# Optimization experiments

Hardware: AMD Instinct MI355X
Metric: run time of the kernel (lower is better)

The kernel has to match this reference:

```python
import jax, jax.numpy as jnp
import numpy as np

IN_SIZE = 128
OUT_SIZE = 128
NEG_SLOPE = 0.01  # flax.nnx.leaky_relu default negative_slope


def setup_inputs() -> dict:
    key = jax.random.key(0)
    x = jax.random.normal(key, (16, IN_SIZE, IN_SIZE, 128), dtype=jnp.float32)
    return {"x": x}


def reference(x) -> jnp.ndarray:
    B, _, _, C = x.shape
    up = jax.image.resize(x, (B, 2 * IN_SIZE, 2 * IN_SIZE, C), method='bilinear', antialias=False)
    # leaky_relu activation on the enlarged intermediate
    act = jnp.where(up >= 0, up, NEG_SLOPE * up)
    # bilinear downsample back to out_size (antialias=False, matching original)
    out = jax.image.resize(act, (B, OUT_SIZE, OUT_SIZE, C), method='bilinear', antialias=False)
    return out
```

## Files before the change

### kernel.cpp

```cpp
#include <hip/hip_runtime.h>


#define NEG_SLOPE 0.01f

__device__ __forceinline__ float lrelu(float v) {
    return fmaxf(v, NEG_SLOPE * v);
}

__device__ __forceinline__ float stencil(float a, float b, float c,
                                         float d, float e, float f,
                                         float g, float h, float i) {
    float up00 = 0.5625f * e + 0.1875f * (b + d) + 0.0625f * a;
    float up01 = 0.5625f * e + 0.1875f * (b + f) + 0.0625f * c;
    float up10 = 0.5625f * e + 0.1875f * (d + h) + 0.0625f * g;
    float up11 = 0.5625f * e + 0.1875f * (f + h) + 0.0625f * i;
    return 0.25f * (lrelu(up00) + lrelu(up01) + lrelu(up10) + lrelu(up11));
}

__global__ __launch_bounds__(256) void ActivationFilter_kernel(
        const float4* __restrict__ in, float4* __restrict__ out) {
    const int idx = blockIdx.x * 256 + threadIdx.x;
    const int c4 = idx & 31;
    const int x  = (idx >> 5) & 127;
    const int y  = (idx >> 12) & 127;
    const int b  = idx >> 19;

    const int xm = max(x - 1, 0), xp = min(x + 1, 127);
    const int ym = max(y - 1, 0), yp = min(y + 1, 127);

    const int rb = b << 7;
#define LD(Y, X) in[((((rb + (Y)) << 7) + (X)) << 5) + c4]
    const float4 A = LD(ym, xm), B = LD(ym, x), C = LD(ym, xp);
    const float4 D = LD(y,  xm), E = LD(y,  x), F = LD(y,  xp);
    const float4 G = LD(yp, xm), H = LD(yp, x), I = LD(yp, xp);
#undef LD

    float4 o;
    o.x = stencil(A.x, B.x, C.x, D.x, E.x, F.x, G.x, H.x, I.x);
    o.y = stencil(A.y, B.y, C.y, D.y, E.y, F.y, G.y, H.y, I.y);
    o.z = stencil(A.z, B.z, C.z, D.z, E.z, F.z, G.z, H.z, I.z);
    o.w = stencil(A.w, B.w, C.w, D.w, E.w, F.w, G.w, H.w, I.w);

    out[idx] = o;
}

extern "C" void kernel_launch(void* const* d_in, const int* in_sizes, int n_in,
                              void* d_out, int out_size, void* d_ws, size_t ws_size,
                              hipStream_t stream) {
    const float4* in = (const float4*)d_in[0];
    float4* out = (float4*)d_out;
    ActivationFilter_kernel<<<dim3(32768), dim3(256), 0, stream>>>(in, out);
}
```

Baseline: 228.3 us.

## Compute 2x2 output pixels per thread to reuse stencil neighborhood loads

Each thread now loads a 4x4 neighborhood of float4 inputs and produces four adjacent output pixels, instead of loading 9 inputs for a single output. This cuts redundant global/cache load traffic per output from 9 to 4 float4 loads. The launch grid shrinks by 4x to match. The cost is higher register use per thread and fewer threads to hide latency.

```diff
diff --git a/kernel.cpp b/kernel.cpp
--- a/kernel.cpp
+++ b/kernel.cpp
@@ -17,31 +17,46 @@
     return 0.25f * (lrelu(up00) + lrelu(up01) + lrelu(up10) + lrelu(up11));
 }
 
+__device__ __forceinline__ float4 stencil4(const float4& a, const float4& b, const float4& c,
+                                           const float4& d, const float4& e, const float4& f,
+                                           const float4& g, const float4& h, const float4& i) {
+    float4 o;
+    o.x = stencil(a.x, b.x, c.x, d.x, e.x, f.x, g.x, h.x, i.x);
+    o.y = stencil(a.y, b.y, c.y, d.y, e.y, f.y, g.y, h.y, i.y);
+    o.z = stencil(a.z, b.z, c.z, d.z, e.z, f.z, g.z, h.z, i.z);
+    o.w = stencil(a.w, b.w, c.w, d.w, e.w, f.w, g.w, h.w, i.w);
+    return o;
+}
+
 __global__ __launch_bounds__(256) void ActivationFilter_kernel(
         const float4* __restrict__ in, float4* __restrict__ out) {
-    const int idx = blockIdx.x * 256 + threadIdx.x;
-    const int c4 = idx & 31;
-    const int x  = (idx >> 5) & 127;
-    const int y  = (idx >> 12) & 127;
-    const int b  = idx >> 19;
+    const int t  = blockIdx.x * 256 + threadIdx.x;
+    const int c4 = t & 31;
+    const int px = (t >> 5) & 63;
+    const int py = (t >> 11) & 63;
+    const int b  = t >> 17;
 
-    const int xm = max(x - 1, 0), xp = min(x + 1, 127);
-    const int ym = max(y - 1, 0), yp = min(y + 1, 127);
+    const int x0 = px << 1, y0 = py << 1;
+    const int xm = max(x0 - 1, 0), x3 = min(x0 + 2, 127);
+    const int ym = max(y0 - 1, 0), y3 = min(y0 + 2, 127);
 
     const int rb = b << 7;
-#define LD(Y, X) in[((((rb + (Y)) << 7) + (X)) << 5) + c4]
-    const float4 A = LD(ym, xm), B = LD(ym, x), C = LD(ym, xp);
-    const float4 D = LD(y,  xm), E = LD(y,  x), F = LD(y,  xp);
-    const float4 G = LD(yp, xm), H = LD(yp, x), I = LD(yp, xp);
-#undef LD
+#define ADDR(Y, X) (((((rb + (Y)) << 7) + (X)) << 5) + c4)
 
-    float4 o;
-    o.x = stencil(A.x, B.x, C.x, D.x, E.x, F.x, G.x, H.x, I.x);
-    o.y = stencil(A.y, B.y, C.y, D.y, E.y, F.y, G.y, H.y, I.y);
-    o.z = stencil(A.z, B.z, C.z, D.z, E.z, F.z, G.z, H.z, I.z);
-    o.w = stencil(A.w, B.w, C.w, D.w, E.w, F.w, G.w, H.w, I.w);
+    const float4 v00 = in[ADDR(ym,   xm)], v01 = in[ADDR(ym,   x0)],
+                 v02 = in[ADDR(ym,   x0+1)], v03 = in[ADDR(ym,   x3)];
+    const float4 v10 = in[ADDR(y0,   xm)], v11 = in[ADDR(y0,   x0)],
+                 v12 = in[ADDR(y0,   x0+1)], v13 = in[ADDR(y0,   x3)];
+    const float4 v20 = in[ADDR(y0+1, xm)], v21 = in[ADDR(y0+1, x0)],
+                 v22 = in[ADDR(y0+1, x0+1)], v23 = in[ADDR(y0+1, x3)];
+    const float4 v30 = in[ADDR(y3,   xm)], v31 = in[ADDR(y3,   x0)],
+                 v32 = in[ADDR(y3,   x0+1)], v33 = in[ADDR(y3,   x3)];
 
-    out[idx] = o;
+    out[ADDR(y0,   x0  )] = stencil4(v00, v01, v02, v10, v11, v12, v20, v21, v22);
+    out[ADDR(y0,   x0+1)] = stencil4(v01, v02, v03, v11, v12, v13, v21, v22, v23);
+    out[ADDR(y0+1, x0  )] = stencil4(v10, v11, v12, v20, v21, v22, v30, v31, v32);
+    out[ADDR(y0+1, x0+1)] = stencil4(v11, v12, v13, v21, v22, v23, v31, v32, v33);
+#undef ADDR
 }
 
 extern "C" void kernel_launch(void* const* d_in, const int* in_sizes, int n_in,
@@ -49,5 +64,5 @@
                               hipStream_t stream) {
     const float4* in = (const float4*)d_in[0];
     float4* out = (float4*)d_out;
-    ActivationFilter_kernel<<<dim3(32768), dim3(256), 0, stream>>>(in, out);
+    ActivationFilter_kernel<<<dim3(8192), dim3(256), 0, stream>>>(in, out);
 }
```

Result: no change. 226.7 us (-0.7%).
